# Kernel optimization log

Measured on AMD Instinct MI355X. Metric: run time of the kernel, lower is better.

The kernel has to match this reference:

```python
import jax, jax.numpy as jnp
import numpy as np

THETA = 10000.0


def apply_rope(x, token_position, theta=THETA):
    # x: [B, H, S, d_k] with interleaved even/odd pairs; token_position: [B, S]
    B, H, S, d_k = x.shape
    inv_freq = 1.0 / theta ** (jnp.arange(0, d_k, 2, dtype=jnp.float32) / d_k)  # [d_k/2]
    angles = token_position.astype(jnp.float32)[:, :, None] * inv_freq[None, None, :]  # [B,S,d_k/2]
    cos = jnp.cos(angles)[:, None, :, :]  # [B,1,S,d_k/2]
    sin = jnp.sin(angles)[:, None, :, :]
    xp = x.reshape(B, H, S, d_k // 2, 2)
    x_even, x_odd = xp[..., 0], xp[..., 1]
    rot_even = x_even * cos - x_odd * sin
    rot_odd = x_even * sin + x_odd * cos
    return jnp.stack([rot_even, rot_odd], axis=-1).reshape(B, H, S, d_k)


def setup_inputs() -> dict:
    key = jax.random.key(0)
    ks = jax.random.split(key, 6)
    B, S, D = 2, 2048, 2048
    x = jax.random.normal(ks[0], (B, S, D), dtype=jnp.float32)
    token_position = jnp.sort(jax.random.randint(ks[1], (B, S), 0, 2048), axis=-1).astype(jnp.int32)
    scale = 0.02
    WQ = jax.random.normal(ks[2], (D, D), dtype=jnp.float32) * scale
    WK = jax.random.normal(ks[3], (D, D), dtype=jnp.float32) * scale
    WV = jax.random.normal(ks[4], (D, D), dtype=jnp.float32) * scale
    WO = jax.random.normal(ks[5], (D, D), dtype=jnp.float32) * scale
    return {"x": x, "token_position": token_position, "WQ": WQ, "WK": WK, "WV": WV, "WO": WO}


def reference(x, token_position, WQ, WK, WV, WO):
    B, S, D = x.shape
    H = 16
    d_k = D // H

    def proj(W):
        return jnp.matmul(x, W).reshape(B, S, H, d_k).transpose(0, 2, 1, 3)  # [B,H,S,d_k]

    Q = apply_rope(proj(WQ), token_position)
    K = apply_rope(proj(WK), token_position)
    V = proj(WV)

    score = jnp.einsum('bhqd,bhkd->bhqk', Q, K) / jnp.sqrt(jnp.float32(d_k))
    causal = jnp.triu(jnp.full((S, S), -jnp.inf, dtype=jnp.float32), k=1)
    score = score + causal
    attn = jax.nn.softmax(score, axis=-1)  # stable max-sub softmax, same math
    out = jnp.einsum('bhqk,bhkd->bhqd', attn, V)
    out = out.transpose(0, 2, 1, 3).reshape(B, S, D)
    return jnp.matmul(out, WO)
```

## Files before the change

kernel.cpp:

```cpp
#include <hip/hip_runtime.h>
#include <hip/hip_bf16.h>
#include <cstdint>
#include <cstddef>

typedef unsigned short u16;
typedef __attribute__((ext_vector_type(4))) unsigned short u16x4;
typedef __attribute__((ext_vector_type(8))) unsigned short u16x8;
typedef __attribute__((ext_vector_type(8))) __bf16 bf16x8;
typedef __attribute__((ext_vector_type(4))) float f32x4;

#define MFMA16(a, b, c) __builtin_amdgcn_mfma_f32_16x16x32_bf16((a), (b), (c), 0, 0, 0)

__device__ __forceinline__ u16 f2bf(float f) {
  uint32_t u = __builtin_bit_cast(uint32_t, f);
  u += 0x7FFFu + ((u >> 16) & 1u);
  return (u16)(u >> 16);
}
__device__ __forceinline__ float bf2f(u16 h) {
  return __builtin_bit_cast(float, (uint32_t)h << 16);
}

typedef const __attribute__((address_space(1))) void gv_t;
typedef __attribute__((address_space(3))) void lv_t;
__device__ __forceinline__ void gload16(const void* g, void* l) {
  __builtin_amdgcn_global_load_lds((gv_t*)g, (lv_t*)l, 16, 0, 0);
}

__global__ void prep(const float* __restrict__ x, const float* __restrict__ w0,
                     const float* __restrict__ w1, const float* __restrict__ w2,
                     const float* __restrict__ w3, u16* __restrict__ xb,
                     u16* __restrict__ wtbase) {
  const int z = blockIdx.z;
  const int bx = blockIdx.x, by = blockIdx.y;
  const int tx = threadIdx.x, ty = threadIdx.y;
  if (z >= 4) {
    const int i = ((z - 4) * 4096 + by * 64 + bx) * 256 + ty * 32 + tx;
    float4 v = ((const float4*)x)[i];
    u16x4 o;
    o[0] = f2bf(v.x); o[1] = f2bf(v.y); o[2] = f2bf(v.z); o[3] = f2bf(v.w);
    ((u16x4*)xb)[i] = o;
    return;
  }
  __shared__ float tile[32][33];
  const float* in = (z == 0) ? w0 : (z == 1) ? w1 : (z == 2) ? w2 : w3;
  u16* out = wtbase + (size_t)z * 4194304;
#pragma unroll
  for (int i = 0; i < 32; i += 8)
    tile[ty + i][tx] = in[(size_t)(by * 32 + ty + i) * 2048 + bx * 32 + tx];
  __syncthreads();
#pragma unroll
  for (int i = 0; i < 32; i += 8)
    out[(size_t)(bx * 32 + ty + i) * 2048 + by * 32 + tx] = f2bf(tile[tx][ty + i]);
}

template <int MODE>
__global__ __launch_bounds__(512, 1) void gemm8(const u16* __restrict__ A,
                                                const u16* __restrict__ Bt,
                                                void* __restrict__ Cv,
                                                const int* __restrict__ pos, int nbn) {
  constexpr int K = 2048;
  __shared__ __align__(16) u16 lds[73728];
  const int tid = threadIdx.x, lane = tid & 63;
  const int lo16 = lane & 15, hi = lane >> 4;
  const int wid = tid >> 6;
  const int wr = wid >> 1, wc = wid & 1;

  const int xcd = (int)blockIdx.x & 7;
  const int idx = (int)blockIdx.x >> 3;
  const int cpx = nbn >> 3;
  const int bn = (xcd * cpx + idx % cpx) * 128;
  const int bm = (idx / cpx) * 256;

  const int srow = tid >> 3;
  const int scol = ((tid & 7) ^ (srow & 7)) * 8;
  const u16* Arow = A + (size_t)(bm + srow) * K + scol;
  const u16* Brow = Bt + (size_t)(bn + srow) * K + scol;
  char* dstbase = (char*)lds + tid * 16;

#define STG_A(qb_, t_, r_) \
  gload16(Arow + (size_t)(r_) * 64 * K + (t_) * 64, dstbase + (qb_) * 49152 + (r_) * 8192)
#define STG_B(qb_, t_, r_) \
  gload16(Brow + (size_t)(r_) * 64 * K + (t_) * 64, dstbase + (qb_) * 49152 + 32768 + (r_) * 8192)

  f32x4 acc[4][4];
  const f32x4 z4 = {0.f, 0.f, 0.f, 0.f};
#pragma unroll
  for (int m = 0; m < 4; ++m)
#pragma unroll
    for (int n = 0; n < 4; ++n) acc[m][n] = z4;

  const int xork = lo16 & 7;
  const int aRow = (wr * 64 + lo16) * 128;
  const int bRow = 32768 + (wc * 64 + lo16) * 128;
  const int x0 = ((hi ^ xork)) << 4;
  const int x1 = (((4 + hi) ^ xork)) << 4;

  STG_A(0, 0, 0); STG_A(0, 0, 1); STG_B(0, 0, 0); STG_A(0, 0, 2); STG_A(0, 0, 3); STG_B(0, 0, 1);
  STG_A(1, 1, 0); STG_A(1, 1, 1); STG_B(1, 1, 0); STG_A(1, 1, 2); STG_A(1, 1, 3); STG_B(1, 1, 1);

  int q = 0;
  for (int t = 0; t < 32; ++t) {
    if (t < 31) {
      asm volatile("s_waitcnt vmcnt(6)" ::: "memory");
    } else {
      asm volatile("s_waitcnt vmcnt(0)" ::: "memory");
    }
    __builtin_amdgcn_s_barrier();
    __builtin_amdgcn_sched_barrier(0);
    const char* Aq = (const char*)lds + q * 49152;
    const int q2 = (q == 0) ? 2 : q - 1;

    bf16x8 b0[4], b1[4], a0[2], a1[2];
#pragma unroll
    for (int n = 0; n < 4; ++n) b0[n] = *(const bf16x8*)(Aq + bRow + n * 2048 + x0);
#pragma unroll
    for (int n = 0; n < 4; ++n) b1[n] = *(const bf16x8*)(Aq + bRow + n * 2048 + x1);
#pragma unroll
    for (int m = 0; m < 2; ++m) a0[m] = *(const bf16x8*)(Aq + aRow + m * 2048 + x0);
#pragma unroll
    for (int m = 0; m < 2; ++m) a1[m] = *(const bf16x8*)(Aq + aRow + m * 2048 + x1);
    if (t < 30) { STG_A(q2, t + 2, 0); STG_A(q2, t + 2, 1); STG_B(q2, t + 2, 0); }
    __builtin_amdgcn_sched_barrier(0);
    __builtin_amdgcn_s_setprio(1);
#pragma unroll
    for (int m = 0; m < 2; ++m)
#pragma unroll
      for (int n = 0; n < 4; ++n) acc[m][n] = MFMA16(a0[m], b0[n], acc[m][n]);
#pragma unroll
    for (int m = 0; m < 2; ++m)
#pragma unroll
      for (int n = 0; n < 4; ++n) acc[m][n] = MFMA16(a1[m], b1[n], acc[m][n]);
    __builtin_amdgcn_s_setprio(0);

    bf16x8 c0[2], c1[2];
#pragma unroll
    for (int m = 0; m < 2; ++m) c0[m] = *(const bf16x8*)(Aq + aRow + (m + 2) * 2048 + x0);
#pragma unroll
    for (int m = 0; m < 2; ++m) c1[m] = *(const bf16x8*)(Aq + aRow + (m + 2) * 2048 + x1);
    if (t < 30) { STG_A(q2, t + 2, 2); STG_A(q2, t + 2, 3); STG_B(q2, t + 2, 1); }
    __builtin_amdgcn_sched_barrier(0);
    __builtin_amdgcn_s_barrier();
    __builtin_amdgcn_sched_barrier(0);
    __builtin_amdgcn_s_setprio(1);
#pragma unroll
    for (int m = 0; m < 2; ++m)
#pragma unroll
      for (int n = 0; n < 4; ++n) acc[m + 2][n] = MFMA16(c0[m], b0[n], acc[m + 2][n]);
#pragma unroll
    for (int m = 0; m < 2; ++m)
#pragma unroll
      for (int n = 0; n < 4; ++n) acc[m + 2][n] = MFMA16(c1[m], b1[n], acc[m + 2][n]);
    __builtin_amdgcn_s_setprio(0);
    q = (q == 2) ? 0 : q + 1;
  }
#undef STG_A
#undef STG_B

  if constexpr (MODE == 2) {
    const int sect = bn >> 11;
    u16* Cq = (u16*)Cv + (size_t)sect * 8388608;
    const int cb = (bn & 2047) + wc * 64;
    if (sect < 2) {
      const float qsc = (sect == 0) ? 0.08838834764831845f : 1.0f;
      float freq[4];
#pragma unroll
      for (int n = 0; n < 4; ++n) {
        const int c = cb + n * 16 + lo16;
        freq[n] = exp2f((float)((c & 127) >> 1) * -0.2076205059304601f);
      }
      const float sg = (lo16 & 1) ? 1.f : -1.f;
#pragma unroll
      for (int m = 0; m < 4; ++m) {
        const int row = bm + wr * 64 + m * 16 + hi * 4;
#pragma unroll
        for (int r = 0; r < 4; ++r) {
          const float p = (float)pos[row + r];
#pragma unroll
          for (int n = 0; n < 4; ++n) {
            const float ang = p * freq[n];
            const float sn = __sinf(ang);
            const float cs = __cosf(ang);
            const float v = acc[m][n][r];
            const float pv = __shfl_xor(v, 1);
            Cq[(size_t)(row + r) * 2048 + cb + n * 16 + lo16] =
                f2bf((v * cs + sg * pv * sn) * qsc);
          }
        }
      }
    } else {
      __syncthreads();
#pragma unroll
      for (int m = 0; m < 4; ++m) {
#pragma unroll
        for (int n = 0; n < 4; ++n) {
          const int d = wc * 64 + n * 16 + lo16;
          const int tokb = wr * 64 + m * 16 + hi * 4;
#pragma unroll
          for (int r = 0; r < 4; ++r)
            lds[d * 260 + tokb + r] = f2bf(acc[m][n][r]);
        }
      }
      __syncthreads();
      const int b = bm >> 11, hh = (bn & 2047) >> 7;
      u16* vt = Cq + ((size_t)((b * 16 + hh) * 128)) * 2048 + (bm & 2047);
#pragma unroll
      for (int j = 0; j < 4; ++j) {
        const int d = (tid >> 4) + j * 32;
        const int t0 = (tid & 15) * 16;
        const u16* src = lds + d * 260 + t0;
        u16* dst = vt + (size_t)d * 2048 + t0;
#pragma unroll
        for (int w = 0; w < 4; ++w)
          *(u16x4*)(dst + w * 4) = *(const u16x4*)(src + w * 4);
      }
    }
  } else {
    float* C = (float*)Cv;
    const int cb = bn + wc * 64;
#pragma unroll
    for (int m = 0; m < 4; ++m)
#pragma unroll
      for (int n = 0; n < 4; ++n)
#pragma unroll
        for (int r = 0; r < 4; ++r)
          C[(size_t)(bm + wr * 64 + m * 16 + hi * 4 + r) * 2048 + cb + n * 16 + lo16] =
              acc[m][n][r];
  }
}

__device__ __forceinline__ void attn_step(const char* Ksc, const char* Vsc, char* Pw,
                                          const bf16x8* qf, f32x4* accO,
                                          float* m_r, float* l_r,
                                          bool diag, int kv0, int qrow0, int lane) {
  const f32x4 z4 = {0.f, 0.f, 0.f, 0.f};
  f32x4 accS[4];
#pragma unroll
  for (int nb = 0; nb < 4; ++nb) accS[nb] = z4;

  __builtin_amdgcn_s_setprio(1);
#pragma unroll
  for (int nb = 0; nb < 4; ++nb) {
    const int kv = nb * 16 + (lane & 15);
#pragma unroll
    for (int kb = 0; kb < 4; ++kb) {
      const int c16 = (kb * 4 + (lane >> 4)) ^ (kv & 7);
      bf16x8 kf = *(const bf16x8*)(Ksc + kv * 256 + c16 * 16);
      accS[nb] = MFMA16(qf[kb], kf, accS[nb]);
    }
  }
  __builtin_amdgcn_s_setprio(0);

  if (diag) {
#pragma unroll
    for (int nb = 0; nb < 4; ++nb) {
      const int kv = kv0 + nb * 16 + (lane & 15);
#pragma unroll
      for (int j = 0; j < 4; ++j)
        if (kv > qrow0 + j) accS[nb][j] = -INFINITY;
    }
  }

  float lm[4];
#pragma unroll
  for (int j = 0; j < 4; ++j)
    lm[j] = fmaxf(fmaxf(accS[0][j], accS[1][j]), fmaxf(accS[2][j], accS[3][j]));
  const bool ok = (lm[0] <= m_r[0] + 8.f) && (lm[1] <= m_r[1] + 8.f) &&
                  (lm[2] <= m_r[2] + 8.f) && (lm[3] <= m_r[3] + 8.f);
  if (!__all(ok)) {
#pragma unroll
    for (int j = 0; j < 4; ++j) {
      float mx = lm[j];
#pragma unroll
      for (int off = 1; off < 16; off <<= 1) mx = fmaxf(mx, __shfl_xor(mx, off));
      const float mn = fmaxf(m_r[j], mx);
      const float sc = __expf(m_r[j] - mn);
      m_r[j] = mn;
      l_r[j] *= sc;
#pragma unroll
      for (int db = 0; db < 8; ++db) accO[db][j] *= sc;
    }
  }

#pragma unroll
  for (int j = 0; j < 4; ++j) {
    float s = 0.f;
#pragma unroll
    for (int nb = 0; nb < 4; ++nb) {
      const float p = __expf(accS[nb][j] - m_r[j]);
      accS[nb][j] = p;
      s += p;
    }
    l_r[j] += s;
    const int ql = (lane >> 4) * 4 + j;
#pragma unroll
    for (int nb = 0; nb < 4; ++nb) {
      const int col = nb * 16 + (lane & 15);
      const int byteoff = ql * 128 + ((((col >> 3) ^ (ql & 7))) << 4) + (col & 7) * 2;
      *(u16*)(Pw + byteoff) = f2bf(accS[nb][j]);
    }
  }

#pragma unroll
  for (int kb2 = 0; kb2 < 2; ++kb2) {
    const int ql = lane & 15;
    const int c16a = (kb2 * 4 + (lane >> 4)) ^ (ql & 7);
    bf16x8 pa = *(const bf16x8*)(Pw + ql * 128 + c16a * 16);
    __builtin_amdgcn_s_setprio(1);
#pragma unroll
    for (int db = 0; db < 8; ++db) {
      const int d = db * 16 + (lane & 15);
      const int c16 = (kb2 * 4 + (lane >> 4)) ^ (d & 7);
      bf16x8 vf = *(const bf16x8*)(Vsc + d * 128 + c16 * 16);
      accO[db] = MFMA16(pa, vf, accO[db]);
    }
    __builtin_amdgcn_s_setprio(0);
  }
}

__global__ __launch_bounds__(256, 2) void flash_attn8(const u16* __restrict__ Qb,
                                                      const u16* __restrict__ Kb,
                                                      const u16* __restrict__ VT,
                                                      u16* __restrict__ Ob) {
  constexpr int S = 2048, HD = 2048;
  const int g = (int)blockIdx.x;
  const int xcd = g & 7, slot = g >> 3;
  const int bh = xcd * 4 + (slot & 3);
  const int pairid = slot >> 2;
  const int b = bh >> 4, h = bh & 15;
  const int tid = threadIdx.x, lane = tid & 63, wid = tid >> 6;
  const int qtA = 31 - pairid, qtB = pairid;
  const int q0a = qtA * 64, q0b = qtB * 64;

  __shared__ u16 Ks[2][64 * 128];
  __shared__ u16 Vs[2][128 * 64];
  __shared__ u16 Ps[4][16 * 64];

  const size_t base = (size_t)b * S * HD + (size_t)h * 128;
  const u16* Qp = Qb + base;
  const u16* Kp = Kb + base;
  const u16* VTp = VT + (size_t)bh * 128 * S;
  u16* Op = Ob + base;

  const f32x4 z4 = {0.f, 0.f, 0.f, 0.f};
  const int kKv = (lane >> 4);
  const int kC16 = (lane & 15);
  const int vD = (lane >> 3);
  const int vC16 = (lane & 7);

#define STAGE(pb, kv0_)                                                                   \
  {                                                                                       \
    _Pragma("unroll") for (int c = 0; c < 4; ++c) {                                       \
      const int ch = wid * 4 + c;                                                         \
      {                                                                                   \
        const int kv = ch * 4 + kKv;                                                      \
        const int c16 = kC16 ^ (kv & 7);                                                  \
        gload16(Kp + (size_t)((kv0_) + kv) * HD + c16 * 8, (char*)Ks[pb] + ch * 1024);    \
      }                                                                                   \
      {                                                                                   \
        const int d = ch * 8 + vD;                                                        \
        const int c16 = vC16 ^ (d & 7);                                                   \
        gload16(VTp + (size_t)d * S + (kv0_) + c16 * 8, (char*)Vs[pb] + ch * 1024);       \
      }                                                                                   \
    }                                                                                     \
  }

  bf16x8 qfA[4], qfB[4];
  {
    const int kc = (lane >> 4) * 8;
    const int qrA = q0a + wid * 16 + (lane & 15);
    const int qrB = q0b + wid * 16 + (lane & 15);
#pragma unroll
    for (int kb = 0; kb < 4; ++kb) {
      qfA[kb] = *(const bf16x8*)(Qp + (size_t)qrA * HD + kb * 32 + kc);
      qfB[kb] = *(const bf16x8*)(Qp + (size_t)qrB * HD + kb * 32 + kc);
    }
  }

  f32x4 accOA[8], accOB[8];
#pragma unroll
  for (int d = 0; d < 8; ++d) { accOA[d] = z4; accOB[d] = z4; }
  float mA[4] = {-INFINITY, -INFINITY, -INFINITY, -INFINITY};
  float lA[4] = {0.f, 0.f, 0.f, 0.f};
  float mB[4] = {-INFINITY, -INFINITY, -INFINITY, -INFINITY};
  float lB[4] = {0.f, 0.f, 0.f, 0.f};

  const int qrow0A = q0a + wid * 16 + (lane >> 4) * 4;
  const int qrow0B = q0b + wid * 16 + (lane >> 4) * 4;
  char* Pw = (char*)&Ps[wid][0];

  STAGE(0, 0);

  for (int t = 0; t <= qtA; ++t) {
    const int cur = t & 1;
    const int kv0 = t * 64;
    if (t < qtA) {
      STAGE(cur ^ 1, kv0 + 64);
      asm volatile("s_waitcnt vmcnt(8)" ::: "memory");
    } else {
      asm volatile("s_waitcnt vmcnt(0)" ::: "memory");
    }
    __builtin_amdgcn_s_barrier();
    __builtin_amdgcn_sched_barrier(0);

    const char* Ksc = (const char*)Ks[cur];
    const char* Vsc = (const char*)Vs[cur];

    attn_step(Ksc, Vsc, Pw, qfA, accOA, mA, lA, t == qtA, kv0, qrow0A, lane);

    if (t <= qtB)
      attn_step(Ksc, Vsc, Pw, qfB, accOB, mB, lB, t == qtB, kv0, qrow0B, lane);

    __builtin_amdgcn_sched_barrier(0);
    __builtin_amdgcn_s_barrier();
  }
#undef STAGE

  float invA[4], invB[4];
#pragma unroll
  for (int j = 0; j < 4; ++j) {
    float la = lA[j], lb = lB[j];
#pragma unroll
    for (int off = 1; off < 16; off <<= 1) {
      la += __shfl_xor(la, off);
      lb += __shfl_xor(lb, off);
    }
    invA[j] = 1.f / la;
    invB[j] = 1.f / lb;
  }
#pragma unroll
  for (int db = 0; db < 8; ++db)
#pragma unroll
    for (int j = 0; j < 4; ++j) {
      const int rowA = qrow0A + j;
      const int rowB = qrow0B + j;
      Op[(size_t)rowA * HD + db * 16 + (lane & 15)] = f2bf(accOA[db][j] * invA[j]);
      Op[(size_t)rowB * HD + db * 16 + (lane & 15)] = f2bf(accOB[db][j] * invB[j]);
    }
}

extern "C" void kernel_launch(void* const* d_in, const int* in_sizes, int n_in,
                              void* d_out, int out_size, void* d_ws, size_t ws_size,
                              hipStream_t stream) {
  const float* x  = (const float*)d_in[0];
  const int*   tp = (const int*)d_in[1];
  const float* WQ = (const float*)d_in[2];
  const float* WK = (const float*)d_in[3];
  const float* WV = (const float*)d_in[4];
  const float* WO = (const float*)d_in[5];

  const size_t MB = 1024 * 1024;
  if (ws_size < 112 * MB) return;
  char* ws = (char*)d_ws;
  u16* xb  = (u16*)(ws + 0 * MB);
  u16* wqt = (u16*)(ws + 16 * MB);
  u16* wot = (u16*)(ws + 40 * MB);
  u16* Qb  = (u16*)(ws + 48 * MB);
  u16* Kb  = (u16*)(ws + 64 * MB);
  u16* VTb = (u16*)(ws + 80 * MB);
  u16* Obf = (u16*)(ws + 96 * MB);

  {
    dim3 g(64, 64, 6), blk(32, 8);
    prep<<<g, blk, 0, stream>>>(x, WQ, WK, WV, WO, xb, wqt);
  }
  gemm8<2><<<768, 512, 0, stream>>>(xb, wqt, (void*)Qb, tp, 48);

  flash_attn8<<<512, 256, 0, stream>>>(Qb, Kb, VTb, Obf);

  gemm8<1><<<256, 512, 0, stream>>>(Obf, wot, d_out, nullptr, 16);
}
```

Baseline: 236.1 us.

## Interleave both query tiles' attention steps and use exp2 softmax with folded log2e

```diff
diff --git a/kernel.cpp b/kernel.cpp
--- a/kernel.cpp
+++ b/kernel.cpp
@@ -161,7 +161,7 @@
     u16* Cq = (u16*)Cv + (size_t)sect * 8388608;
     const int cb = (bn & 2047) + wc * 64;
     if (sect < 2) {
-      const float qsc = (sect == 0) ? 0.08838834764831845f : 1.0f;
+      const float qsc = (sect == 0) ? 0.12751743f : 1.0f;
       float freq[4];
 #pragma unroll
       for (int n = 0; n < 4; ++n) {
@@ -228,44 +228,14 @@
   }
 }
 
-__device__ __forceinline__ void attn_step(const char* Ksc, const char* Vsc, char* Pw,
-                                          const bf16x8* qf, f32x4* accO,
-                                          float* m_r, float* l_r,
-                                          bool diag, int kv0, int qrow0, int lane) {
-  const f32x4 z4 = {0.f, 0.f, 0.f, 0.f};
-  f32x4 accS[4];
-#pragma unroll
-  for (int nb = 0; nb < 4; ++nb) accS[nb] = z4;
-
-  __builtin_amdgcn_s_setprio(1);
-#pragma unroll
-  for (int nb = 0; nb < 4; ++nb) {
-    const int kv = nb * 16 + (lane & 15);
-#pragma unroll
-    for (int kb = 0; kb < 4; ++kb) {
-      const int c16 = (kb * 4 + (lane >> 4)) ^ (kv & 7);
-      bf16x8 kf = *(const bf16x8*)(Ksc + kv * 256 + c16 * 16);
-      accS[nb] = MFMA16(qf[kb], kf, accS[nb]);
-    }
-  }
-  __builtin_amdgcn_s_setprio(0);
-
-  if (diag) {
-#pragma unroll
-    for (int nb = 0; nb < 4; ++nb) {
-      const int kv = kv0 + nb * 16 + (lane & 15);
-#pragma unroll
-      for (int j = 0; j < 4; ++j)
-        if (kv > qrow0 + j) accS[nb][j] = -INFINITY;
-    }
-  }
-
+__device__ __forceinline__ void sm_write(f32x4* accS, float* m_r, float* l_r,
+                                         f32x4* accO, char* Pw, int lane) {
   float lm[4];
 #pragma unroll
   for (int j = 0; j < 4; ++j)
     lm[j] = fmaxf(fmaxf(accS[0][j], accS[1][j]), fmaxf(accS[2][j], accS[3][j]));
-  const bool ok = (lm[0] <= m_r[0] + 8.f) && (lm[1] <= m_r[1] + 8.f) &&
-                  (lm[2] <= m_r[2] + 8.f) && (lm[3] <= m_r[3] + 8.f);
+  const bool ok = (lm[0] <= m_r[0] + 11.5f) && (lm[1] <= m_r[1] + 11.5f) &&
+                  (lm[2] <= m_r[2] + 11.5f) && (lm[3] <= m_r[3] + 11.5f);
   if (!__all(ok)) {
 #pragma unroll
     for (int j = 0; j < 4; ++j) {
@@ -273,51 +243,30 @@
 #pragma unroll
       for (int off = 1; off < 16; off <<= 1) mx = fmaxf(mx, __shfl_xor(mx, off));
       const float mn = fmaxf(m_r[j], mx);
-      const float sc = __expf(m_r[j] - mn);
+      const float sc = exp2f(m_r[j] - mn);
       m_r[j] = mn;
       l_r[j] *= sc;
 #pragma unroll
       for (int db = 0; db < 8; ++db) accO[db][j] *= sc;
     }
   }
-
 #pragma unroll
   for (int j = 0; j < 4; ++j) {
     float s = 0.f;
+    const int ql = (lane >> 4) * 4 + j;
 #pragma unroll
     for (int nb = 0; nb < 4; ++nb) {
-      const float p = __expf(accS[nb][j] - m_r[j]);
-      accS[nb][j] = p;
+      const float p = exp2f(accS[nb][j] - m_r[j]);
       s += p;
-    }
-    l_r[j] += s;
-    const int ql = (lane >> 4) * 4 + j;
-#pragma unroll
-    for (int nb = 0; nb < 4; ++nb) {
       const int col = nb * 16 + (lane & 15);
       const int byteoff = ql * 128 + ((((col >> 3) ^ (ql & 7))) << 4) + (col & 7) * 2;
-      *(u16*)(Pw + byteoff) = f2bf(accS[nb][j]);
-    }
-  }
-
-#pragma unroll
-  for (int kb2 = 0; kb2 < 2; ++kb2) {
-    const int ql = lane & 15;
-    const int c16a = (kb2 * 4 + (lane >> 4)) ^ (ql & 7);
-    bf16x8 pa = *(const bf16x8*)(Pw + ql * 128 + c16a * 16);
-    __builtin_amdgcn_s_setprio(1);
-#pragma unroll
-    for (int db = 0; db < 8; ++db) {
-      const int d = db * 16 + (lane & 15);
-      const int c16 = (kb2 * 4 + (lane >> 4)) ^ (d & 7);
-      bf16x8 vf = *(const bf16x8*)(Vsc + d * 128 + c16 * 16);
-      accO[db] = MFMA16(pa, vf, accO[db]);
-    }
-    __builtin_amdgcn_s_setprio(0);
-  }
-}
-
-__global__ __launch_bounds__(256, 2) void flash_attn8(const u16* __restrict__ Qb,
+      *(u16*)(Pw + byteoff) = (u16)(__builtin_bit_cast(uint32_t, p) >> 16);
+    }
+    l_r[j] += s;
+  }
+}
+
+__global__ __launch_bounds__(256, 2) void flash_attn9(const u16* __restrict__ Qb,
                                                       const u16* __restrict__ Kb,
                                                       const u16* __restrict__ VT,
                                                       u16* __restrict__ Ob) {
@@ -333,7 +282,7 @@
 
   __shared__ u16 Ks[2][64 * 128];
   __shared__ u16 Vs[2][128 * 64];
-  __shared__ u16 Ps[4][16 * 64];
+  __shared__ u16 Ps[4][2][16 * 64];
 
   const size_t base = (size_t)b * S * HD + (size_t)h * 128;
   const u16* Qp = Qb + base;
@@ -386,11 +335,75 @@
 
   const int qrow0A = q0a + wid * 16 + (lane >> 4) * 4;
   const int qrow0B = q0b + wid * 16 + (lane >> 4) * 4;
-  char* Pw = (char*)&Ps[wid][0];
+  char* Pw0 = (char*)&Ps[wid][0][0];
+  char* Pw1 = (char*)&Ps[wid][1][0];
 
   STAGE(0, 0);
 
-  for (int t = 0; t <= qtA; ++t) {
+  int t = 0;
+  for (; t <= qtB; ++t) {
+    const int cur = t & 1;
+    const int kv0 = t * 64;
+    STAGE(cur ^ 1, kv0 + 64);
+    asm volatile("s_waitcnt vmcnt(8)" ::: "memory");
+    __builtin_amdgcn_s_barrier();
+    __builtin_amdgcn_sched_barrier(0);
+
+    const char* Ksc = (const char*)Ks[cur];
+    const char* Vsc = (const char*)Vs[cur];
+
+    f32x4 sA[4], sB[4];
+#pragma unroll
+    for (int nb = 0; nb < 4; ++nb) { sA[nb] = z4; sB[nb] = z4; }
+    __builtin_amdgcn_s_setprio(1);
+#pragma unroll
+    for (int nb = 0; nb < 4; ++nb) {
+      const int kv = nb * 16 + (lane & 15);
+#pragma unroll
+      for (int kb = 0; kb < 4; ++kb) {
+        const int c16 = (kb * 4 + (lane >> 4)) ^ (kv & 7);
+        bf16x8 kf = *(const bf16x8*)(Ksc + kv * 256 + c16 * 16);
+        sA[nb] = MFMA16(qfA[kb], kf, sA[nb]);
+        sB[nb] = MFMA16(qfB[kb], kf, sB[nb]);
+      }
+    }
+    __builtin_amdgcn_s_setprio(0);
+
+    if (t == qtB) {
+#pragma unroll
+      for (int nb = 0; nb < 4; ++nb) {
+        const int kv = kv0 + nb * 16 + (lane & 15);
+#pragma unroll
+        for (int j = 0; j < 4; ++j)
+          if (kv > qrow0B + j) sB[nb][j] = -INFINITY;
+      }
+    }
+
+    sm_write(sA, mA, lA, accOA, Pw0, lane);
+    sm_write(sB, mB, lB, accOB, Pw1, lane);
+
+#pragma unroll
+    for (int kb2 = 0; kb2 < 2; ++kb2) {
+      const int ql = lane & 15;
+      const int c16a = (kb2 * 4 + (lane >> 4)) ^ (ql & 7);
+      bf16x8 paA = *(const bf16x8*)(Pw0 + ql * 128 + c16a * 16);
+      bf16x8 paB = *(const bf16x8*)(Pw1 + ql * 128 + c16a * 16);
+      __builtin_amdgcn_s_setprio(1);
+#pragma unroll
+      for (int db = 0; db < 8; ++db) {
+        const int d = db * 16 + (lane & 15);
+        const int c16 = (kb2 * 4 + (lane >> 4)) ^ (d & 7);
+        bf16x8 vf = *(const bf16x8*)(Vsc + d * 128 + c16 * 16);
+        accOA[db] = MFMA16(paA, vf, accOA[db]);
+        accOB[db] = MFMA16(paB, vf, accOB[db]);
+      }
+      __builtin_amdgcn_s_setprio(0);
+    }
+    __builtin_amdgcn_sched_barrier(0);
+    __builtin_amdgcn_s_barrier();
+  }
+
+  for (; t <= qtA; ++t) {
     const int cur = t & 1;
     const int kv0 = t * 64;
     if (t < qtA) {
@@ -405,11 +418,49 @@
     const char* Ksc = (const char*)Ks[cur];
     const char* Vsc = (const char*)Vs[cur];
 
-    attn_step(Ksc, Vsc, Pw, qfA, accOA, mA, lA, t == qtA, kv0, qrow0A, lane);
-
-    if (t <= qtB)
-      attn_step(Ksc, Vsc, Pw, qfB, accOB, mB, lB, t == qtB, kv0, qrow0B, lane);
-
+    f32x4 sA[4];
+#pragma unroll
+    for (int nb = 0; nb < 4; ++nb) sA[nb] = z4;
+    __builtin_amdgcn_s_setprio(1);
+#pragma unroll
+    for (int nb = 0; nb < 4; ++nb) {
+      const int kv = nb * 16 + (lane & 15);
+#pragma unroll
+      for (int kb = 0; kb < 4; ++kb) {
+        const int c16 = (kb * 4 + (lane >> 4)) ^ (kv & 7);
+        bf16x8 kf = *(const bf16x8*)(Ksc + kv * 256 + c16 * 16);
+        sA[nb] = MFMA16(qfA[kb], kf, sA[nb]);
+      }
+    }
+    __builtin_amdgcn_s_setprio(0);
+
+    if (t == qtA) {
+#pragma unroll
+      for (int nb = 0; nb < 4; ++nb) {
+        const int kv = kv0 + nb * 16 + (lane & 15);
+#pragma unroll
+        for (int j = 0; j < 4; ++j)
+          if (kv > qrow0A + j) sA[nb][j] = -INFINITY;
+      }
+    }
+
+    sm_write(sA, mA, lA, accOA, Pw0, lane);
+
+#pragma unroll
+    for (int kb2 = 0; kb2 < 2; ++kb2) {
+      const int ql = lane & 15;
+      const int c16a = (kb2 * 4 + (lane >> 4)) ^ (ql & 7);
+      bf16x8 paA = *(const bf16x8*)(Pw0 + ql * 128 + c16a * 16);
+      __builtin_amdgcn_s_setprio(1);
+#pragma unroll
+      for (int db = 0; db < 8; ++db) {
+        const int d = db * 16 + (lane & 15);
+        const int c16 = (kb2 * 4 + (lane >> 4)) ^ (d & 7);
+        bf16x8 vf = *(const bf16x8*)(Vsc + d * 128 + c16 * 16);
+        accOA[db] = MFMA16(paA, vf, accOA[db]);
+      }
+      __builtin_amdgcn_s_setprio(0);
+    }
     __builtin_amdgcn_sched_barrier(0);
     __builtin_amdgcn_s_barrier();
   }
@@ -465,7 +516,7 @@
   }
   gemm8<2><<<768, 512, 0, stream>>>(xb, wqt, (void*)Qb, tp, 48);
 
-  flash_attn8<<<512, 256, 0, stream>>>(Qb, Kb, VTb, Obf);
+  flash_attn9<<<512, 256, 0, stream>>>(Qb, Kb, VTb, Obf);
 
   gemm8<1><<<256, 512, 0, stream>>>(Obf, wot, d_out, nullptr, 16);
 }
```

After: 236.9 us. No clear change (+0.3%).
